# Optimization experiments

Hardware: AMD Instinct MI355X
Metric: run time of the kernel (lower is better)

## Reference

```python
import math
import jax, jax.numpy as jnp
import numpy as np

N_EMBED = 1024
N_HEAD = 16
B, T = 2, 2048


def _gelu_tanh(x):
    # GPT-2 tanh-approx GELU
    c = math.sqrt(2.0 / math.pi)
    return 0.5 * x * (1.0 + jnp.tanh(c * (x + 0.044715 * x * x * x)))


def _layer_norm(x, w, b, eps=1e-5):
    mu = jnp.mean(x, axis=-1, keepdims=True)
    var = jnp.var(x, axis=-1, keepdims=True)
    return (x - mu) * jax.lax.rsqrt(var + eps) * w + b


def setup_inputs() -> dict:
    key = jax.random.key(0)
    ks = jax.random.split(key, 8)
    s = lambda fan_in: 1.0 / math.sqrt(fan_in)
    return {
        "x": jax.random.normal(ks[0], (B, T, N_EMBED), jnp.float32),
        "ln1_w": jnp.ones((N_EMBED,), jnp.float32),
        "ln1_b": jnp.zeros((N_EMBED,), jnp.float32),
        "W_attn": jax.random.normal(ks[1], (N_EMBED, 3 * N_EMBED), jnp.float32) * s(N_EMBED),
        "b_attn": jnp.zeros((3 * N_EMBED,), jnp.float32),
        "W_o": jax.random.normal(ks[2], (N_EMBED, N_EMBED), jnp.float32) * s(N_EMBED),
        "b_o": jnp.zeros((N_EMBED,), jnp.float32),
        "ln2_w": jnp.ones((N_EMBED,), jnp.float32),
        "ln2_b": jnp.zeros((N_EMBED,), jnp.float32),
        "W_fc": jax.random.normal(ks[3], (N_EMBED, 4 * N_EMBED), jnp.float32) * s(N_EMBED),
        "b_fc": jnp.zeros((4 * N_EMBED,), jnp.float32),
        "W_proj": jax.random.normal(ks[4], (4 * N_EMBED, N_EMBED), jnp.float32) * s(4 * N_EMBED),
        "b_proj": jnp.zeros((N_EMBED,), jnp.float32),
    }


def reference(x, ln1_w, ln1_b, W_attn, b_attn, W_o, b_o,
              ln2_w, ln2_b, W_fc, b_fc, W_proj, b_proj):
    Bx, Tx, C = x.shape
    H = N_HEAD
    Dh = C // H

    # --- attention ---
    h = _layer_norm(x, ln1_w, ln1_b)
    qkv = h @ W_attn + b_attn                       # [B,T,3C]
    q, k, v = jnp.split(qkv, 3, axis=-1)
    q = q.reshape(Bx, Tx, H, Dh).transpose(0, 2, 1, 3)   # [B,H,T,Dh]
    k = k.reshape(Bx, Tx, H, Dh).transpose(0, 2, 1, 3)
    v = v.reshape(Bx, Tx, H, Dh).transpose(0, 2, 1, 3)

    attn = jnp.einsum("bhqd,bhkd->bhqk", q, k) * (1.0 / math.sqrt(Dh))
    causal = jnp.tril(jnp.ones((Tx, Tx), dtype=bool))
    attn = jnp.where(causal[None, None], attn, -jnp.inf)
    attn = jax.nn.softmax(attn, axis=-1)
    y = jnp.einsum("bhqk,bhkd->bhqd", attn, v)      # [B,H,T,Dh]
    y = y.transpose(0, 2, 1, 3).reshape(Bx, Tx, C)
    y = y @ W_o + b_o
    x = x + y

    # --- MLP ---
    h = _layer_norm(x, ln2_w, ln2_b)
    h = _gelu_tanh(h @ W_fc + b_fc)
    h = h @ W_proj + b_proj
    return x + h
```

## Files before the change

### kernel.cpp

```cpp
#include <hip/hip_runtime.h>
#include <math.h>

constexpr int TDIM = 2048;
constexpr int BDIM = 2;
constexpr int CDIM = 1024;
constexpr int HEADS = 16;
constexpr int DH = 64;
constexpr int MDIM = BDIM * TDIM;

typedef short bf16x8 __attribute__((ext_vector_type(8)));
typedef float f32x4 __attribute__((ext_vector_type(4)));
typedef float f32x16 __attribute__((ext_vector_type(16)));

__device__ __forceinline__ float b2f(unsigned short u) {
    union { float f; unsigned int i; } v; v.i = ((unsigned int)u) << 16; return v.f;
}
__device__ __forceinline__ unsigned short f2b(float f) {
    union { float f; unsigned int i; } v; v.f = f;
    unsigned int r = (v.i + 0x7FFFu + ((v.i >> 16) & 1u)) >> 16;
    return (unsigned short)r;
}
__device__ __forceinline__ unsigned int cvtpk(float lo, float hi) {
    unsigned int r;
    asm("v_cvt_pk_bf16_f32 %0, %1, %2" : "=v"(r) : "v"(lo), "v"(hi));
    return r;
}
__device__ __forceinline__ float gelu_f(float x) {
    float z = -2.3022077f * (x + 0.044715f * x * x * x);
    return x / (1.0f + exp2f(z));
}
__device__ __forceinline__ void async_copy16(const void* g, void* l) {
    __builtin_amdgcn_global_load_lds(
        (const __attribute__((address_space(1))) unsigned int*)g,
        (__attribute__((address_space(3))) unsigned int*)l, 16, 0, 0);
}

__global__ __launch_bounds__(256) void transpose_cast(
    const float* __restrict__ W, unsigned short* __restrict__ Wt, int K, int N) {
    __shared__ float tile[32][33];
    int n0 = blockIdx.x * 32, k0 = blockIdx.y * 32;
    int tx = threadIdx.x & 31, ty = threadIdx.x >> 5;
#pragma unroll
    for (int i = 0; i < 32; i += 8)
        tile[ty + i][tx] = W[(size_t)(k0 + ty + i) * N + n0 + tx];
    __syncthreads();
#pragma unroll
    for (int i = 0; i < 32; i += 8)
        Wt[(size_t)(n0 + ty + i) * K + k0 + tx] = f2b(tile[tx][ty + i]);
}

__global__ __launch_bounds__(256) void ln_kernel(
    const float* __restrict__ x, const float* __restrict__ w,
    const float* __restrict__ b, unsigned short* __restrict__ out) {
    int row = blockIdx.x;
    int tid = threadIdx.x;
    const float* xr = x + (size_t)row * CDIM;
    float4 v = *(const float4*)(xr + tid * 4);
    float s  = v.x + v.y + v.z + v.w;
    float ss = v.x * v.x + v.y * v.y + v.z * v.z + v.w * v.w;
#pragma unroll
    for (int off = 32; off >= 1; off >>= 1) {
        s  += __shfl_xor(s, off);
        ss += __shfl_xor(ss, off);
    }
    __shared__ float rs[4], rss[4];
    int wave = tid >> 6;
    if ((tid & 63) == 0) { rs[wave] = s; rss[wave] = ss; }
    __syncthreads();
    s  = rs[0] + rs[1] + rs[2] + rs[3];
    ss = rss[0] + rss[1] + rss[2] + rss[3];
    float mean = s * (1.0f / CDIM);
    float var  = ss * (1.0f / CDIM) - mean * mean;
    float rstd = rsqrtf(var + 1e-5f);
    float4 wv = *(const float4*)(w + tid * 4);
    float4 bv = *(const float4*)(b + tid * 4);
    ushort4 o;
    o.x = f2b((v.x - mean) * rstd * wv.x + bv.x);
    o.y = f2b((v.y - mean) * rstd * wv.y + bv.y);
    o.z = f2b((v.z - mean) * rstd * wv.z + bv.z);
    o.w = f2b((v.w - mean) * rstd * wv.w + bv.w);
    *(ushort4*)(out + (size_t)row * CDIM + tid * 4) = o;
}

template <int MODE, int BN, int NBUF>
__global__ __launch_bounds__(256) void gemm_bf16(
    const unsigned short* __restrict__ A, const unsigned short* __restrict__ Wt,
    const float* __restrict__ bias, const float* __restrict__ res,
    void* __restrict__ Cout, int M, int N, int K) {
    constexpr int JF = BN / 32;
    constexpr int INF = 4 + JF;
    __shared__ __align__(16) short As[NBUF][128 * 64];
    __shared__ __align__(16) short Bs[NBUF][BN * 64];
    const int tid = threadIdx.x;
    const int lane = tid & 63, w = tid >> 6;
    const int wr = w >> 1, wc = w & 1;

    const int nwg = gridDim.x * gridDim.y;
    const int bid = blockIdx.y * gridDim.x + blockIdx.x;
    const int nbid = (bid & 7) * (nwg >> 3) + (bid >> 3);
    const int bx = nbid % gridDim.x;
    const int by = nbid / gridDim.x;
    const int row0 = by * 128, col0 = bx * BN;

    const int sr = lane >> 3;
    const int sc = 8 * ((lane & 7) ^ sr);
    const unsigned short* gA = A  + (size_t)(row0 + w * 8 + sr) * K + sc;
    const unsigned short* gB = Wt + (size_t)(col0 + w * 8 + sr) * K + sc;

    f32x4 acc[4][JF] = {};
    const int h = lane >> 4;
    const int r15 = lane & 15;
    const int nt = K >> 6;

#pragma unroll
    for (int pt = 0; pt < NBUF - 1; ++pt) {
        const int kp = pt << 6;
#pragma unroll
        for (int i = 0; i < 4; ++i)
            async_copy16(gA + (size_t)i * 32 * K + kp, &As[pt][(w * 8 + i * 32) * 64]);
#pragma unroll
        for (int i = 0; i < JF; ++i)
            async_copy16(gB + (size_t)i * 32 * K + kp, &Bs[pt][(w * 8 + i * 32) * 64]);
    }

    for (int t = 0; t < nt; ++t) {
        const int cur = t % NBUF;
        const int tp = t + NBUF - 1;
        if (tp < nt) {
            const int bufp = tp % NBUF;
            const int kp = tp << 6;
#pragma unroll
            for (int i = 0; i < 4; ++i)
                async_copy16(gA + (size_t)i * 32 * K + kp, &As[bufp][(w * 8 + i * 32) * 64]);
#pragma unroll
            for (int i = 0; i < JF; ++i)
                async_copy16(gB + (size_t)i * 32 * K + kp, &Bs[bufp][(w * 8 + i * 32) * 64]);
            asm volatile("s_waitcnt vmcnt(%0)" :: "n"((NBUF - 1) * INF) : "memory");
        } else {
            asm volatile("s_waitcnt vmcnt(0)" ::: "memory");
        }
        __builtin_amdgcn_s_barrier();
        asm volatile("" ::: "memory");

#pragma unroll
        for (int ks = 0; ks < 2; ++ks) {
            bf16x8 af[4], bfr[JF];
#pragma unroll
            for (int i = 0; i < 4; ++i) {
                int ra = wr * 64 + i * 16 + r15;
                int offa = ra * 128 + ((ks * 64 + h * 16) ^ ((ra & 7) << 4));
                af[i] = *(const bf16x8*)((const char*)As[cur] + offa);
            }
#pragma unroll
            for (int j = 0; j < JF; ++j) {
                int rb = wc * (BN / 2) + j * 16 + r15;
                int offb = rb * 128 + ((ks * 64 + h * 16) ^ ((rb & 7) << 4));
                bfr[j] = *(const bf16x8*)((const char*)Bs[cur] + offb);
            }
#pragma unroll
            for (int i = 0; i < 4; ++i)
#pragma unroll
                for (int j = 0; j < JF; ++j)
                    acc[i][j] = __builtin_amdgcn_mfma_f32_16x16x32_bf16(
                        af[i], bfr[j], acc[i][j], 0, 0, 0);
        }
        asm volatile("" ::: "memory");
        __builtin_amdgcn_s_barrier();
    }

#pragma unroll
    for (int i = 0; i < 4; ++i) {
#pragma unroll
        for (int j = 0; j < JF; ++j) {
            int c = col0 + wc * (BN / 2) + j * 16 + r15;
            float bv = bias[c];
#pragma unroll
            for (int q = 0; q < 4; ++q) {
                int rr = row0 + wr * 64 + i * 16 + h * 4 + q;
                float v = acc[i][j][q] + bv;
                if (MODE == 2) v = gelu_f(v);
                if (MODE == 1) v += res[(size_t)rr * N + c];
                if (MODE == 1) ((float*)Cout)[(size_t)rr * N + c] = v;
                else ((unsigned short*)Cout)[(size_t)rr * N + c] = f2b(v);
            }
        }
    }
}

__global__ __launch_bounds__(512, 4) void attn_mfma(
    const unsigned short* __restrict__ qkv, unsigned short* __restrict__ y) {
    const int bh = blockIdx.x;
    const int b = bh >> 4, hh = bh & 15;
    const int by = blockIdx.y;
    const int qy = (by < 8) ? (15 - by) : (by - 8);
    const int q0 = qy * 128;
    const int tid = threadIdx.x;
    const int lane = tid & 63, w = tid >> 6;
    const int p = w & 3, half = w >> 2;
    const int hi = lane >> 5, q31 = lane & 31;

    const float SC  = 0.1803368801111244f;
    const float THR = 44.0f;

    __shared__ __align__(16) char smem[36864];
    float (*Os)[68] = (float (*)[68])smem;
    float* mlm = (float*)(smem + 34816);
    float* mll = (float*)(smem + 34816 + 1024);

    const size_t base = (size_t)b * TDIM * (3 * CDIM);
    const unsigned short* qb = qkv + base + hh * DH;
    const unsigned short* kb = qkv + base + CDIM + hh * DH;
    const unsigned short* vb = qkv + base + 2 * CDIM + hh * DH;

    const int gq = q0 + p * 32 + q31;
    const int qmin_w = q0 + p * 32;
    const int qmax_w = qmin_w + 31;

    bf16x8 qf[4];
#pragma unroll
    for (int ks = 0; ks < 4; ++ks)
        qf[ks] = *(const bf16x8*)(qb + (size_t)gq * (3 * CDIM) + ks * 16 + hi * 8);

    const int sr = lane >> 3;
    const int scK = 8 * ((lane & 7) ^ sr);
    const int rV = tid >> 3;
    const int dblk = (tid & 7) * 8;

    f32x16 oacc[2] = {};
    float m = -1e30f, l = 0.f;
    bf16x8 vreg;

    const int NT = 2 * qy + 2;

    {
        short* Ks0 = (short*)smem;
        int rowbase = w * 8;
        async_copy16(kb + (size_t)(rowbase + sr) * (3 * CDIM) + scK, Ks0 + rowbase * 64);
        vreg = *(const bf16x8*)(vb + (size_t)rV * (3 * CDIM) + dblk);
        char* Vt0 = smem + 16384;
#pragma unroll
        for (int j = 0; j < 8; ++j) {
            int d = dblk + j;
            int swz = ((d ^ (d >> 3)) & 7) << 4;
            *(short*)(Vt0 + d * 128 + ((2 * rV) ^ swz)) = vreg[j];
        }
    }
    __syncthreads();

    for (int kt = 0; kt < NT; ++kt) {
        const int c = kt & 1;
        const char* Ksc = smem + c * 8192;
        const char* Vtc = smem + 16384 + c * 8192;
        const bool pre = (kt + 1 < NT);

        if (pre) {
            const int kv1 = (kt + 1) * 64;
            short* Ksn = (short*)(smem + (c ^ 1) * 8192);
            int rowbase = w * 8;
            async_copy16(kb + (size_t)(kv1 + rowbase + sr) * (3 * CDIM) + scK,
                         Ksn + rowbase * 64);
            vreg = *(const bf16x8*)(vb + (size_t)(kv1 + rV) * (3 * CDIM) + dblk);
        }

        const int kvs = kt * 64 + half * 32;
        if (kvs <= qmax_w) {
            f32x16 sacc = {};
            __builtin_amdgcn_s_setprio(1);
#pragma unroll
            for (int ks = 0; ks < 4; ++ks) {
                int row = half * 32 + q31;
                int off = row * 128 + ((32 * ks + 16 * hi) ^ ((row & 7) << 4));
                bf16x8 kf = *(const bf16x8*)(Ksc + off);
                sacc = __builtin_amdgcn_mfma_f32_32x32x16_bf16(kf, qf[ks], sacc, 0, 0, 0);
            }
            __builtin_amdgcn_s_setprio(0);

            float p_[16];
            if (kvs + 31 > qmin_w) {
#pragma unroll
                for (int r = 0; r < 16; ++r) {
                    int kvg = kvs + (r & 3) + 8 * (r >> 2) + 4 * hi;
                    p_[r] = (kvg > gq) ? -1e30f : sacc[r];
                }
            } else {
#pragma unroll
                for (int r = 0; r < 16; ++r) p_[r] = sacc[r];
            }

            float t8[8];
#pragma unroll
            for (int r = 0; r < 8; ++r) t8[r] = fmaxf(p_[r], p_[r + 8]);
#pragma unroll
            for (int r = 0; r < 4; ++r) t8[r] = fmaxf(t8[r], t8[r + 4]);
            float pm = fmaxf(fmaxf(t8[0], t8[1]), fmaxf(t8[2], t8[3]));
            pm = fmaxf(pm, __shfl_xor(pm, 32));

            if (!__all(pm <= m + THR)) {
                float mnew = fmaxf(m, pm);
                float sf = exp2f((m - mnew) * SC);
                m = mnew;
                l *= sf;
                oacc[0] *= sf;
                oacc[1] *= sf;
            }
            float mc = m * SC;
#pragma unroll
            for (int r = 0; r < 16; ++r) p_[r] = exp2f(fmaf(p_[r], SC, -mc));
#pragma unroll
            for (int r = 0; r < 8; ++r) t8[r] = p_[r] + p_[r + 8];
#pragma unroll
            for (int r = 0; r < 4; ++r) t8[r] = t8[r] + t8[r + 4];
            float rsum = (t8[0] + t8[1]) + (t8[2] + t8[3]);
            rsum += __shfl_xor(rsum, 32);
            l += rsum;

            bf16x8 pa[2];
#pragma unroll
            for (int k2 = 0; k2 < 2; ++k2) {
                unsigned int A0 = cvtpk(p_[8 * k2 + 0], p_[8 * k2 + 1]);
                unsigned int A1 = cvtpk(p_[8 * k2 + 2], p_[8 * k2 + 3]);
                unsigned int B0 = cvtpk(p_[8 * k2 + 4], p_[8 * k2 + 5]);
                unsigned int B1 = cvtpk(p_[8 * k2 + 6], p_[8 * k2 + 7]);
                unsigned int sA0 = __shfl_xor((int)A0, 32);
                unsigned int sA1 = __shfl_xor((int)A1, 32);
                unsigned int sB0 = __shfl_xor((int)B0, 32);
                unsigned int sB1 = __shfl_xor((int)B1, 32);
                union { int i[4]; bf16x8 h; } u;
                u.i[0] = hi ? (int)sB0 : (int)A0;
                u.i[1] = hi ? (int)sB1 : (int)A1;
                u.i[2] = hi ? (int)B0 : (int)sA0;
                u.i[3] = hi ? (int)B1 : (int)sA1;
                pa[k2] = u.h;
            }

            __builtin_amdgcn_s_setprio(1);
#pragma unroll
            for (int j2 = 0; j2 < 2; ++j2) {
                int row = 32 * j2 + q31;
                int swz = ((row ^ (row >> 3)) & 7) << 4;
#pragma unroll
                for (int k2 = 0; k2 < 2; ++k2) {
                    int off = row * 128 + ((64 * half + 32 * k2 + 16 * hi) ^ swz);
                    bf16x8 vf = *(const bf16x8*)(Vtc + off);
                    oacc[j2] = __builtin_amdgcn_mfma_f32_32x32x16_bf16(vf, pa[k2], oacc[j2], 0, 0, 0);
                }
            }
            __builtin_amdgcn_s_setprio(0);
        }

        if (pre) {
            char* Vtn = smem + 16384 + (c ^ 1) * 8192;
#pragma unroll
            for (int j = 0; j < 8; ++j) {
                int d = dblk + j;
                int swz = ((d ^ (d >> 3)) & 7) << 4;
                *(short*)(Vtn + d * 128 + ((2 * rV) ^ swz)) = vreg[j];
            }
        }
        __syncthreads();
    }

    mlm[(half * 4 + p) * 32 + q31] = m;
    mll[(half * 4 + p) * 32 + q31] = l;
    __syncthreads();
    float mo = mlm[((half ^ 1) * 4 + p) * 32 + q31];
    float lo = mll[((half ^ 1) * 4 + p) * 32 + q31];
    float M  = fmaxf(m, mo);
    float sf  = exp2f((m - M) * SC);
    float sfo = exp2f((mo - M) * SC);
    float invl = 1.0f / (l * sf + lo * sfo);

    if (half == 1) {
#pragma unroll
        for (int j2 = 0; j2 < 2; ++j2)
#pragma unroll
            for (int g = 0; g < 4; ++g) {
                float4 v4 = make_float4(oacc[j2][4 * g + 0] * sf, oacc[j2][4 * g + 1] * sf,
                                        oacc[j2][4 * g + 2] * sf, oacc[j2][4 * g + 3] * sf);
                *(float4*)&Os[p * 32 + q31][32 * j2 + 8 * g + 4 * hi] = v4;
            }
    }
    __syncthreads();
    if (half == 0) {
#pragma unroll
        for (int j2 = 0; j2 < 2; ++j2)
#pragma unroll
            for (int g = 0; g < 4; ++g) {
                float4 t = *(const float4*)&Os[p * 32 + q31][32 * j2 + 8 * g + 4 * hi];
                float4 v4;
                v4.x = (oacc[j2][4 * g + 0] * sf + t.x) * invl;
                v4.y = (oacc[j2][4 * g + 1] * sf + t.y) * invl;
                v4.z = (oacc[j2][4 * g + 2] * sf + t.z) * invl;
                v4.w = (oacc[j2][4 * g + 3] * sf + t.w) * invl;
                *(float4*)&Os[p * 32 + q31][32 * j2 + 8 * g + 4 * hi] = v4;
            }
    }
    __syncthreads();

    const int r0 = tid >> 4;
    const int c4 = (tid & 15) * 4;
#pragma unroll
    for (int pass = 0; pass < 4; ++pass) {
        int row = pass * 32 + r0;
        float4 v = *(const float4*)&Os[row][c4];
        ushort4 o;
        o.x = f2b(v.x); o.y = f2b(v.y); o.z = f2b(v.z); o.w = f2b(v.w);
        *(ushort4*)(y + (size_t)(b * TDIM + q0 + row) * CDIM + hh * DH + c4) = o;
    }
}

extern "C" void kernel_launch(void* const* d_in, const int* in_sizes, int n_in,
                              void* d_out, int out_size, void* d_ws, size_t ws_size,
                              hipStream_t stream) {
    const float* x      = (const float*)d_in[0];
    const float* ln1_w  = (const float*)d_in[1];
    const float* ln1_b  = (const float*)d_in[2];
    const float* W_attn = (const float*)d_in[3];
    const float* b_attn = (const float*)d_in[4];
    const float* W_o    = (const float*)d_in[5];
    const float* b_o    = (const float*)d_in[6];
    const float* ln2_w  = (const float*)d_in[7];
    const float* ln2_b  = (const float*)d_in[8];
    const float* W_fc   = (const float*)d_in[9];
    const float* b_fc   = (const float*)d_in[10];
    const float* W_proj = (const float*)d_in[11];
    const float* b_proj = (const float*)d_in[12];
    float* out = (float*)d_out;

    char* ws = (char*)d_ws;
    const size_t MB = 1024 * 1024;
    unsigned short* h_bf    = (unsigned short*)(ws);
    unsigned short* big     = (unsigned short*)(ws + 8 * MB);
    unsigned short* Wt_attn = (unsigned short*)(ws + 40 * MB);
    unsigned short* Wt_o    = (unsigned short*)(ws + 46 * MB);
    unsigned short* Wt_fc   = (unsigned short*)(ws + 48 * MB);
    unsigned short* Wt_proj = (unsigned short*)(ws + 56 * MB);
    float* x1 = out;

    hipLaunchKernelGGL(transpose_cast, dim3(96, 32),  dim3(256), 0, stream, W_attn, Wt_attn, CDIM, 3 * CDIM);
    hipLaunchKernelGGL(transpose_cast, dim3(32, 32),  dim3(256), 0, stream, W_o,    Wt_o,    CDIM, CDIM);
    hipLaunchKernelGGL(transpose_cast, dim3(128, 32), dim3(256), 0, stream, W_fc,   Wt_fc,   CDIM, 4 * CDIM);
    hipLaunchKernelGGL(transpose_cast, dim3(32, 128), dim3(256), 0, stream, W_proj, Wt_proj, 4 * CDIM, CDIM);

    hipLaunchKernelGGL(ln_kernel, dim3(MDIM), dim3(256), 0, stream, x, ln1_w, ln1_b, h_bf);
    hipLaunchKernelGGL((gemm_bf16<0, 128, 2>), dim3(3 * CDIM / 128, MDIM / 128), dim3(256), 0,
                       stream, h_bf, Wt_attn, b_attn, nullptr, big, MDIM, 3 * CDIM, CDIM);
    hipLaunchKernelGGL(attn_mfma, dim3(BDIM * HEADS, TDIM / 128), dim3(512), 0, stream,
                       big, h_bf);
    hipLaunchKernelGGL((gemm_bf16<1, 64, 3>), dim3(CDIM / 64, MDIM / 128), dim3(256), 0,
                       stream, h_bf, Wt_o, b_o, x, x1, MDIM, CDIM, CDIM);
    hipLaunchKernelGGL(ln_kernel, dim3(MDIM), dim3(256), 0, stream, x1, ln2_w, ln2_b, h_bf);
    hipLaunchKernelGGL((gemm_bf16<2, 128, 2>), dim3(4 * CDIM / 128, MDIM / 128), dim3(256), 0,
                       stream, h_bf, Wt_fc, b_fc, nullptr, big, MDIM, 4 * CDIM, CDIM);
    hipLaunchKernelGGL((gemm_bf16<1, 64, 3>), dim3(CDIM / 64, MDIM / 128), dim3(256), 0,
                       stream, big, Wt_proj, b_proj, x1, out, MDIM, CDIM, 4 * CDIM);
}
```

Before: 239.4 us.

## Add 256x256-tile ping-pong GEMM kernel for QKV and FC projections

Introduces a 512-thread GEMM with 256x256 output tiles, double-buffered async global-to-LDS loads and swizzled LDS reads. It interleaves MFMA phases with explicit barriers and priority boosts, and uses it for the QKV and MLP-up GEMMs. The larger tile raises arithmetic intensity and cuts redundant global reads. In exchange the grid shrinks to roughly one wave of large blocks, and LDS use per block is high, which limits occupancy.

```diff
diff --git a/kernel.cpp b/kernel.cpp
--- a/kernel.cpp
+++ b/kernel.cpp
@@ -34,6 +34,10 @@
         (const __attribute__((address_space(1))) unsigned int*)g,
         (__attribute__((address_space(3))) unsigned int*)l, 16, 0, 0);
 }
+
+#define PBAR do { asm volatile("" ::: "memory"); __builtin_amdgcn_s_barrier(); \
+                  asm volatile("" ::: "memory"); } while (0)
+#define LGKM0 asm volatile("s_waitcnt lgkmcnt(0)" ::: "memory")
 
 __global__ __launch_bounds__(256) void transpose_cast(
     const float* __restrict__ W, unsigned short* __restrict__ Wt, int K, int N) {
@@ -82,6 +86,138 @@
     *(ushort4*)(out + (size_t)row * CDIM + tid * 4) = o;
 }
 
+template <int MODE>
+__global__ __launch_bounds__(512, 2) void gemm256(
+    const unsigned short* __restrict__ A, const unsigned short* __restrict__ Wt,
+    const float* __restrict__ bias, void* __restrict__ Cout, int M, int N, int K) {
+    __shared__ __align__(16) short As[2][256 * 64];
+    __shared__ __align__(16) short Bs[2][256 * 64];
+    const int tid = threadIdx.x;
+    const int lane = tid & 63, w = tid >> 6;
+    const int wm = w >> 2, wn = w & 3;
+    const int h = lane >> 4, r15 = lane & 15;
+    const int sr = lane >> 3;
+    const int sc = 8 * ((lane & 7) ^ sr);
+
+    const int nwg = gridDim.x * gridDim.y;
+    const int bid = blockIdx.y * gridDim.x + blockIdx.x;
+    const int nbid = (bid & 7) * (nwg >> 3) + (bid >> 3);
+    const int bx = nbid % gridDim.x;
+    const int by = nbid / gridDim.x;
+    const int row0 = by * 256, col0 = bx * 256;
+
+    const unsigned short* gA = A  + (size_t)(row0 + w * 8 + sr) * K + sc;
+    const unsigned short* gB = Wt + (size_t)(col0 + w * 8 + sr) * K + sc;
+
+    f32x4 acc[8][4] = {};
+    bf16x8 aA[4][2], bB[4][2];
+
+    auto stA = [&](int kt, int hh) {
+        short* dst = &As[kt & 1][(hh * 128 + w * 8) * 64];
+        const unsigned short* src = gA + (size_t)(hh * 128) * K + (size_t)kt * 64;
+        async_copy16(src, dst);
+        async_copy16(src + (size_t)64 * K, dst + 64 * 64);
+    };
+    auto stB = [&](int kt, int hh) {
+        short* dst = &Bs[kt & 1][(hh * 128 + w * 8) * 64];
+        const unsigned short* src = gB + (size_t)(hh * 128) * K + (size_t)kt * 64;
+        async_copy16(src, dst);
+        async_copy16(src + (size_t)64 * K, dst + 64 * 64);
+    };
+    auto rdA = [&](const short* S, int rh) {
+#pragma unroll
+        for (int ii = 0; ii < 4; ++ii)
+#pragma unroll
+            for (int ks = 0; ks < 2; ++ks) {
+                int ra = wm * 128 + rh * 64 + ii * 16 + r15;
+                int off = ra * 128 + ((ks * 64 + h * 16) ^ ((ra & 7) << 4));
+                aA[ii][ks] = *(const bf16x8*)((const char*)S + off);
+            }
+    };
+    auto rdB = [&](const short* S, int J0) {
+#pragma unroll
+        for (int dj = 0; dj < 2; ++dj)
+#pragma unroll
+            for (int ks = 0; ks < 2; ++ks) {
+                int rb = wn * 64 + (J0 + dj) * 16 + r15;
+                int off = rb * 128 + ((ks * 64 + h * 16) ^ ((rb & 7) << 4));
+                bB[J0 + dj][ks] = *(const bf16x8*)((const char*)S + off);
+            }
+    };
+    auto mm = [&](int rh, int ch) {
+        __builtin_amdgcn_s_setprio(1);
+#pragma unroll
+        for (int ii = 0; ii < 4; ++ii)
+#pragma unroll
+            for (int jj = 0; jj < 2; ++jj)
+#pragma unroll
+                for (int ks = 0; ks < 2; ++ks)
+                    acc[rh * 4 + ii][ch * 2 + jj] = __builtin_amdgcn_mfma_f32_16x16x32_bf16(
+                        aA[ii][ks], bB[ch * 2 + jj][ks], acc[rh * 4 + ii][ch * 2 + jj], 0, 0, 0);
+        __builtin_amdgcn_s_setprio(0);
+    };
+
+    const int niter = K >> 7;
+
+    stA(0, 0); stB(0, 0); stB(0, 1); stA(0, 1);
+    stA(1, 0); stB(1, 0); stB(1, 1);
+    asm volatile("s_waitcnt vmcnt(6)" ::: "memory");
+    PBAR;
+
+    for (int t = 0; t < niter; ++t) {
+        const bool st = (t + 1 < niter);
+        const int t2 = 2 * t + 2, t3 = 2 * t + 3;
+        rdA(As[0], 0); rdB(Bs[0], 0);
+        stA(2 * t + 1, 1);
+        PBAR; LGKM0; mm(0, 0); PBAR;
+        rdB(Bs[0], 2);
+        PBAR; LGKM0; mm(0, 1); PBAR;
+        rdA(As[0], 1);
+        if (st) stB(t2, 0);
+        PBAR; LGKM0; mm(1, 0); PBAR;
+        if (st) {
+            stB(t2, 1);
+            stA(t2, 0);
+            asm volatile("s_waitcnt vmcnt(6)" ::: "memory");
+        } else {
+            asm volatile("s_waitcnt vmcnt(0)" ::: "memory");
+        }
+        PBAR; LGKM0; mm(1, 1); PBAR;
+        rdA(As[1], 0); rdB(Bs[1], 0);
+        if (st) stA(t2, 1);
+        PBAR; LGKM0; mm(0, 0); PBAR;
+        rdB(Bs[1], 2);
+        PBAR; LGKM0; mm(0, 1); PBAR;
+        rdA(As[1], 1);
+        if (st) stB(t3, 0);
+        PBAR; LGKM0; mm(1, 0); PBAR;
+        if (st) {
+            stB(t3, 1);
+            stA(t3, 0);
+            asm volatile("s_waitcnt vmcnt(6)" ::: "memory");
+        } else {
+            asm volatile("s_waitcnt vmcnt(0)" ::: "memory");
+        }
+        PBAR; LGKM0; mm(1, 1); PBAR;
+    }
+
+#pragma unroll
+    for (int I = 0; I < 8; ++I) {
+#pragma unroll
+        for (int J = 0; J < 4; ++J) {
+            int cc = col0 + wn * 64 + J * 16 + r15;
+            float bv = bias[cc];
+#pragma unroll
+            for (int q = 0; q < 4; ++q) {
+                int rr = row0 + wm * 128 + I * 16 + h * 4 + q;
+                float v = acc[I][J][q] + bv;
+                if (MODE == 2) v = gelu_f(v);
+                ((unsigned short*)Cout)[(size_t)rr * N + cc] = f2b(v);
+            }
+        }
+    }
+}
+
 template <int MODE, int BN, int NBUF>
 __global__ __launch_bounds__(256) void gemm_bf16(
     const unsigned short* __restrict__ A, const unsigned short* __restrict__ Wt,
@@ -443,15 +579,15 @@
     hipLaunchKernelGGL(transpose_cast, dim3(32, 128), dim3(256), 0, stream, W_proj, Wt_proj, 4 * CDIM, CDIM);
 
     hipLaunchKernelGGL(ln_kernel, dim3(MDIM), dim3(256), 0, stream, x, ln1_w, ln1_b, h_bf);
-    hipLaunchKernelGGL((gemm_bf16<0, 128, 2>), dim3(3 * CDIM / 128, MDIM / 128), dim3(256), 0,
-                       stream, h_bf, Wt_attn, b_attn, nullptr, big, MDIM, 3 * CDIM, CDIM);
+    hipLaunchKernelGGL((gemm256<0>), dim3(3 * CDIM / 256, MDIM / 256), dim3(512), 0,
+                       stream, h_bf, Wt_attn, b_attn, big, MDIM, 3 * CDIM, CDIM);
     hipLaunchKernelGGL(attn_mfma, dim3(BDIM * HEADS, TDIM / 128), dim3(512), 0, stream,
                        big, h_bf);
     hipLaunchKernelGGL((gemm_bf16<1, 64, 3>), dim3(CDIM / 64, MDIM / 128), dim3(256), 0,
                        stream, h_bf, Wt_o, b_o, x, x1, MDIM, CDIM, CDIM);
     hipLaunchKernelGGL(ln_kernel, dim3(MDIM), dim3(256), 0, stream, x1, ln2_w, ln2_b, h_bf);
-    hipLaunchKernelGGL((gemm_bf16<2, 128, 2>), dim3(4 * CDIM / 128, MDIM / 128), dim3(256), 0,
-                       stream, h_bf, Wt_fc, b_fc, nullptr, big, MDIM, 4 * CDIM, CDIM);
+    hipLaunchKernelGGL((gemm256<2>), dim3(4 * CDIM / 256, MDIM / 256), dim3(512), 0,
+                       stream, h_bf, Wt_fc, b_fc, big, MDIM, 4 * CDIM, CDIM);
     hipLaunchKernelGGL((gemm_bf16<1, 64, 3>), dim3(CDIM / 64, MDIM / 128), dim3(256), 0,
                        stream, big, Wt_proj, b_proj, x1, out, MDIM, CDIM, 4 * CDIM);
 }
```

New measurement: 236.1 us. About the same (-1.4%).
